# Kernel tuning notes

Measured on AMD Instinct MI355X. Metric: run time of the kernel, lower is better.

The kernel has to match this reference:

```python
import jax, jax.numpy as jnp
import numpy as np

N = 2048   # num_params = feature dim = number of ring Givens angles
B = 16384  # batch


def setup_inputs() -> dict:
    key = jax.random.key(0)
    k1, k2 = jax.random.split(key)
    x = jax.random.normal(k1, (B, N), dtype=jnp.float32)
    angles = jax.random.normal(k2, (N,), dtype=jnp.float32)
    return {"x": x, "angles": angles}


def _build_rotation(angles):
    """R = G_0 @ G_1 @ ... @ G_{n-1}, built by sequential right-multiplication.

    Right-multiplying M by Givens G_k (plane (i, j)=(k, (k+1)%n), angle theta_k,
    with G[i,i]=c, G[j,i]=s, G[i,j]=-s, G[j,j]=c) only mixes columns i and j:
        new_col_i =  c*col_i + s*col_j
        new_col_j = -s*col_i + c*col_j
    This is O(n) per step -> O(n^2) total, identical math to the original
    O(n^4) loop of full n x n matmuls against per-step identity matrices.
    """
    n = angles.shape[0]
    idx_i = jnp.arange(n)
    idx_j = (idx_i + 1) % n

    def step(M, inp):
        theta, i, j = inp
        c = jnp.cos(theta)
        s = jnp.sin(theta)
        col_i = M[:, i]
        col_j = M[:, j]
        M = M.at[:, i].set(c * col_i + s * col_j)
        M = M.at[:, j].set(-s * col_i + c * col_j)
        return M, None

    M0 = jnp.eye(n, dtype=angles.dtype)
    R, _ = jax.lax.scan(step, M0, (angles, idx_i, idx_j))
    return R


def reference(x, angles):
    R = _build_rotation(angles)   # [N, N], orthogonal (product of Givens)
    return x @ R.T                # [B, N]
```

## Files before the change

kernel.cpp:

```cpp
#include <hip/hip_runtime.h>
#include <stdint.h>

#define NN  2048
#define SEG 32
#define QPS 8
#define QPR 512
#define WPB 8
#define RPW 4

#define GLOBAL_AS __attribute__((address_space(1)))
#define LDS_AS    __attribute__((address_space(3)))

__global__ __launch_bounds__(512, 4) void ring_givens_scan_kernel(
        const float* __restrict__ x,
        const float* __restrict__ angles,
        float* __restrict__ y,
        int B) {
    __shared__ float4 csT2[SEG / 2][64];
    __shared__ float4 buf[WPB][QPR];
    const int tid  = threadIdx.x;
    const int lane = tid & 63;
    const int wib  = tid >> 6;
    float4* wl = buf[wib];

    {
        float4 av = ((const float4*)angles)[tid];
        float c0, s0, c1, s1, c2, s2, c3, s3;
        sincosf(av.x, &s0, &c0);
        sincosf(av.y, &s1, &c1);
        sincosf(av.z, &s2, &c2);
        sincosf(av.w, &s3, &c3);
        csT2[2 * (tid & 7)    ][tid >> 3] = make_float4(c0, s0, c1, s1);
        csT2[2 * (tid & 7) + 1][tid >> 3] = make_float4(c2, s2, c3, s3);
    }
    __syncthreads();

    const float4 csE = csT2[15][63];
    const float cl = csE.z, sl = csE.w;

    float Mseg = 1.0f;
    #pragma unroll
    for (int q = 0; q < QPS; ++q) {
        float4 A  = csT2[2 * q    ][lane];
        float4 Bq = csT2[2 * q + 1][lane];
        Mseg *= (A.y * A.w) * (Bq.y * Bq.w);
    }
    float Ms[6];
    float Mc = Mseg;
    #pragma unroll
    for (int d = 1, st = 0; d < 64; d <<= 1, ++st) {
        Ms[st] = (lane + d < 64) ? Mc : 0.0f;
        float Mo = __shfl_down(Mc, d);
        if (lane + d < 64) Mc = Mc * Mo;
    }
    float Mn = __shfl_down(Mc, 1);
    Mn = (lane == 63) ? 1.0f : Mn;

    const int gwid        = blockIdx.x * WPB + wib;
    const int total_waves = gridDim.x * WPB;

    for (int r = 0; r < RPW; ++r) {
        const int row = gwid + r * total_waves;
        if (row >= B) break;
        const float4* __restrict__ xr4 = (const float4*)(x + (size_t)row * NN);
        float4*       __restrict__ yr4 = (float4*)      (y + (size_t)row * NN);

        #pragma unroll
        for (int t = 0; t < 8; ++t) {
            const int srcq = (t * 64 + lane) ^ ((lane >> 3) & 7);
            __builtin_amdgcn_global_load_lds(
                (const GLOBAL_AS uint32_t*)(const void*)(xr4 + srcq),
                (LDS_AS uint32_t*)(void*)(wl + t * 64), 16, 0, 0);
        }
        asm volatile("s_waitcnt vmcnt(0)" ::: "memory");

        const float x0v = ((const float*)wl)[0];
        const float xlv = ((const float*)wl)[504 * 4 + 3];
        const float t0  = sl * xlv + cl * x0v;
        if (lane == 0) ((float*)wl)[0] = t0;

        float U = 0.0f;
        #pragma unroll
        for (int q = QPS - 1; q >= 0; --q) {
            float4 v  = wl[lane * QPS + (q ^ (lane & 7))];
            float4 A  = csT2[2 * q    ][lane];
            float4 Bq = csT2[2 * q + 1][lane];
            U = Bq.z * v.w - Bq.w * U;
            U = Bq.x * v.z - Bq.y * U;
            U = A.z  * v.y - A.w  * U;
            U = A.x  * v.x - A.y  * U;
        }

        #pragma unroll
        for (int d = 1, st = 0; d < 64; d <<= 1, ++st) {
            float Uo = __shfl_down(U, d);
            U = fmaf(Ms[st], Uo, U);
        }
        float Un = __shfl_down(U, 1);
        Un = (lane == 63) ? 0.0f : Un;
        float a = fmaf(Mn, x0v, Un);

        const int segq = lane * QPS;
        float e31, p0, p1, p2;
        {
            float4 v  = wl[segq + (7 ^ (lane & 7))];
            float4 A  = csT2[14][lane];
            float4 Bq = csT2[15][lane];
            e31 = Bq.w * v.w + Bq.z * a;  a = Bq.z * v.w - Bq.w * a;
            p2  = Bq.y * v.z + Bq.x * a;  a = Bq.x * v.z - Bq.y * a;
            p1  = A.w  * v.y + A.z  * a;  a = A.z  * v.y - A.w  * a;
            p0  = A.y  * v.x + A.x  * a;  a = A.x  * v.x - A.y  * a;
        }
        #pragma unroll
        for (int q = QPS - 2; q >= 0; --q) {
            float4 v  = wl[segq + (q ^ (lane & 7))];
            float4 A  = csT2[2 * q    ][lane];
            float4 Bq = csT2[2 * q + 1][lane];
            float e3 = Bq.w * v.w + Bq.z * a;  a = Bq.z * v.w - Bq.w * a;
            wl[segq + ((q + 1) ^ (lane & 7))] = make_float4(e3, p0, p1, p2);
            float e2 = Bq.y * v.z + Bq.x * a;  a = Bq.x * v.z - Bq.y * a;
            float e1 = A.w  * v.y + A.z  * a;  a = A.z  * v.y - A.w  * a;
            float e0 = A.y  * v.x + A.x  * a;  a = A.x  * v.x - A.y  * a;
            p0 = e0; p1 = e1; p2 = e2;
        }
        float prev = __shfl_up(e31, 1);
        float s0v  = (lane == 0) ? a : prev;
        wl[segq + (0 ^ (lane & 7))] = make_float4(s0v, p0, p1, p2);

        #pragma unroll
        for (int t = 0; t < 8; ++t) {
            const int p = t * 64 + lane;
            float4 v = wl[p ^ ((lane >> 3) & 7)];
            yr4[p] = v;
        }
        asm volatile("s_waitcnt lgkmcnt(0)" ::: "memory");
    }
}

extern "C" void kernel_launch(void* const* d_in, const int* in_sizes, int n_in,
                              void* d_out, int out_size, void* d_ws, size_t ws_size,
                              hipStream_t stream) {
    const float* x      = (const float*)d_in[0];
    const float* angles = (const float*)d_in[1];
    float* y            = (float*)d_out;

    const int B = in_sizes[0] / NN;
    const int total_waves = (B + RPW - 1) / RPW;
    const int blocks = (total_waves + WPB - 1) / WPB;
    hipLaunchKernelGGL(ring_givens_scan_kernel, dim3(blocks), dim3(512), 0, stream,
                       x, angles, y, B);
}
```

Measured before the change: 249.3 us.

## Double-buffer row loads into LDS and keep cos/sin coefficients in registers

Each wave now prefetches the next row into a second LDS buffer with async global-to-LDS loads while it computes the current row, so load latency overlaps with the scan. Cos/sin coefficients are computed per lane into registers instead of a shared LDS table, which removes the __syncthreads and the repeated LDS reads; the row segment is also read once into registers. The block shrinks to 4 waves and each wave handles 8 rows. This raises register pressure and LDS per wave, and relies on the vmcnt(8) count matching the store/load ordering; the trailing lgkmcnt wait was removed while LDS is reused across iterations.

```diff
diff --git a/kernel.cpp b/kernel.cpp
--- a/kernel.cpp
+++ b/kernel.cpp
@@ -2,49 +2,45 @@
 #include <stdint.h>
 
 #define NN  2048
-#define SEG 32
 #define QPS 8
 #define QPR 512
-#define WPB 8
-#define RPW 4
+#define WPB 4
+#define RPW 8
 
 #define GLOBAL_AS __attribute__((address_space(1)))
 #define LDS_AS    __attribute__((address_space(3)))
 
-__global__ __launch_bounds__(512, 4) void ring_givens_scan_kernel(
+__global__ __launch_bounds__(256, 2) void ring_givens_scan_kernel(
         const float* __restrict__ x,
         const float* __restrict__ angles,
         float* __restrict__ y,
         int B) {
-    __shared__ float4 csT2[SEG / 2][64];
-    __shared__ float4 buf[WPB][QPR];
-    const int tid  = threadIdx.x;
-    const int lane = tid & 63;
-    const int wib  = tid >> 6;
-    float4* wl = buf[wib];
+    __shared__ float4 buf[WPB][2][QPR];
+    const int lane = threadIdx.x & 63;
+    const int wib  = threadIdx.x >> 6;
+    float4* b0 = buf[wib][0];
+    float4* b1 = buf[wib][1];
 
+    float4 A[QPS], Bq[QPS];
     {
-        float4 av = ((const float4*)angles)[tid];
-        float c0, s0, c1, s1, c2, s2, c3, s3;
-        sincosf(av.x, &s0, &c0);
-        sincosf(av.y, &s1, &c1);
-        sincosf(av.z, &s2, &c2);
-        sincosf(av.w, &s3, &c3);
-        csT2[2 * (tid & 7)    ][tid >> 3] = make_float4(c0, s0, c1, s1);
-        csT2[2 * (tid & 7) + 1][tid >> 3] = make_float4(c2, s2, c3, s3);
+        const float4* ap4 = (const float4*)(angles + lane * 32);
+        #pragma unroll
+        for (int q = 0; q < QPS; ++q) {
+            float4 av = ap4[q];
+            float ss, cc;
+            sincosf(av.x, &ss, &cc); A[q].x = cc;  A[q].y = ss;
+            sincosf(av.y, &ss, &cc); A[q].z = cc;  A[q].w = ss;
+            sincosf(av.z, &ss, &cc); Bq[q].x = cc; Bq[q].y = ss;
+            sincosf(av.w, &ss, &cc); Bq[q].z = cc; Bq[q].w = ss;
+        }
     }
-    __syncthreads();
-
-    const float4 csE = csT2[15][63];
-    const float cl = csE.z, sl = csE.w;
+    float sl, cl;
+    sincosf(angles[NN - 1], &sl, &cl);
 
     float Mseg = 1.0f;
     #pragma unroll
-    for (int q = 0; q < QPS; ++q) {
-        float4 A  = csT2[2 * q    ][lane];
-        float4 Bq = csT2[2 * q + 1][lane];
-        Mseg *= (A.y * A.w) * (Bq.y * Bq.w);
-    }
+    for (int q = 0; q < QPS; ++q)
+        Mseg *= (A[q].y * A[q].w) * (Bq[q].y * Bq[q].w);
     float Ms[6];
     float Mc = Mseg;
     #pragma unroll
@@ -59,36 +55,56 @@
     const int gwid        = blockIdx.x * WPB + wib;
     const int total_waves = gridDim.x * WPB;
 
-    for (int r = 0; r < RPW; ++r) {
-        const int row = gwid + r * total_waves;
-        if (row >= B) break;
-        const float4* __restrict__ xr4 = (const float4*)(x + (size_t)row * NN);
-        float4*       __restrict__ yr4 = (float4*)      (y + (size_t)row * NN);
-
+    if (gwid < B) {
+        const float4* xr4 = (const float4*)(x + (size_t)gwid * NN);
         #pragma unroll
         for (int t = 0; t < 8; ++t) {
             const int srcq = (t * 64 + lane) ^ ((lane >> 3) & 7);
             __builtin_amdgcn_global_load_lds(
                 (const GLOBAL_AS uint32_t*)(const void*)(xr4 + srcq),
-                (LDS_AS uint32_t*)(void*)(wl + t * 64), 16, 0, 0);
+                (LDS_AS uint32_t*)(void*)(b0 + t * 64), 16, 0, 0);
         }
-        asm volatile("s_waitcnt vmcnt(0)" ::: "memory");
+    }
 
-        const float x0v = ((const float*)wl)[0];
-        const float xlv = ((const float*)wl)[504 * 4 + 3];
+    for (int r = 0; r < RPW; ++r) {
+        const int row = gwid + r * total_waves;
+        if (row >= B) break;
+        float4* P = (r & 1) ? b1 : b0;
+        float4* Q = (r & 1) ? b0 : b1;
+
+        if (r == 0) asm volatile("s_waitcnt vmcnt(0)" ::: "memory");
+        else        asm volatile("s_waitcnt vmcnt(8)" ::: "memory");
+
+        const int nrow = row + total_waves;
+        if (r + 1 < RPW && nrow < B) {
+            const float4* xn4 = (const float4*)(x + (size_t)nrow * NN);
+            #pragma unroll
+            for (int t = 0; t < 8; ++t) {
+                const int srcq = (t * 64 + lane) ^ ((lane >> 3) & 7);
+                __builtin_amdgcn_global_load_lds(
+                    (const GLOBAL_AS uint32_t*)(const void*)(xn4 + srcq),
+                    (LDS_AS uint32_t*)(void*)(Q + t * 64), 16, 0, 0);
+            }
+        }
+
+        const int segq = lane * QPS;
+        float4 w4[QPS];
+        #pragma unroll
+        for (int q = 0; q < QPS; ++q)
+            w4[q] = P[segq + (q ^ (lane & 7))];
+
+        const float x0v = __shfl(w4[0].x, 0);
+        const float xlv = __shfl(w4[7].w, 63);
         const float t0  = sl * xlv + cl * x0v;
-        if (lane == 0) ((float*)wl)[0] = t0;
+        if (lane == 0) w4[0].x = t0;
 
         float U = 0.0f;
         #pragma unroll
         for (int q = QPS - 1; q >= 0; --q) {
-            float4 v  = wl[lane * QPS + (q ^ (lane & 7))];
-            float4 A  = csT2[2 * q    ][lane];
-            float4 Bq = csT2[2 * q + 1][lane];
-            U = Bq.z * v.w - Bq.w * U;
-            U = Bq.x * v.z - Bq.y * U;
-            U = A.z  * v.y - A.w  * U;
-            U = A.x  * v.x - A.y  * U;
+            U = Bq[q].z * w4[q].w - Bq[q].w * U;
+            U = Bq[q].x * w4[q].z - Bq[q].y * U;
+            U = A[q].z  * w4[q].y - A[q].w  * U;
+            U = A[q].x  * w4[q].x - A[q].y  * U;
         }
 
         #pragma unroll
@@ -100,40 +116,35 @@
         Un = (lane == 63) ? 0.0f : Un;
         float a = fmaf(Mn, x0v, Un);
 
-        const int segq = lane * QPS;
         float e31, p0, p1, p2;
         {
-            float4 v  = wl[segq + (7 ^ (lane & 7))];
-            float4 A  = csT2[14][lane];
-            float4 Bq = csT2[15][lane];
-            e31 = Bq.w * v.w + Bq.z * a;  a = Bq.z * v.w - Bq.w * a;
-            p2  = Bq.y * v.z + Bq.x * a;  a = Bq.x * v.z - Bq.y * a;
-            p1  = A.w  * v.y + A.z  * a;  a = A.z  * v.y - A.w  * a;
-            p0  = A.y  * v.x + A.x  * a;  a = A.x  * v.x - A.y  * a;
+            float4 v = w4[7];
+            e31 = Bq[7].w * v.w + Bq[7].z * a;  a = Bq[7].z * v.w - Bq[7].w * a;
+            p2  = Bq[7].y * v.z + Bq[7].x * a;  a = Bq[7].x * v.z - Bq[7].y * a;
+            p1  = A[7].w  * v.y + A[7].z  * a;  a = A[7].z  * v.y - A[7].w  * a;
+            p0  = A[7].y  * v.x + A[7].x  * a;  a = A[7].x  * v.x - A[7].y  * a;
         }
         #pragma unroll
         for (int q = QPS - 2; q >= 0; --q) {
-            float4 v  = wl[segq + (q ^ (lane & 7))];
-            float4 A  = csT2[2 * q    ][lane];
-            float4 Bq = csT2[2 * q + 1][lane];
-            float e3 = Bq.w * v.w + Bq.z * a;  a = Bq.z * v.w - Bq.w * a;
-            wl[segq + ((q + 1) ^ (lane & 7))] = make_float4(e3, p0, p1, p2);
-            float e2 = Bq.y * v.z + Bq.x * a;  a = Bq.x * v.z - Bq.y * a;
-            float e1 = A.w  * v.y + A.z  * a;  a = A.z  * v.y - A.w  * a;
-            float e0 = A.y  * v.x + A.x  * a;  a = A.x  * v.x - A.y  * a;
+            float4 v = w4[q];
+            float e3 = Bq[q].w * v.w + Bq[q].z * a;  a = Bq[q].z * v.w - Bq[q].w * a;
+            P[segq + ((q + 1) ^ (lane & 7))] = make_float4(e3, p0, p1, p2);
+            float e2 = Bq[q].y * v.z + Bq[q].x * a;  a = Bq[q].x * v.z - Bq[q].y * a;
+            float e1 = A[q].w  * v.y + A[q].z  * a;  a = A[q].z  * v.y - A[q].w  * a;
+            float e0 = A[q].y  * v.x + A[q].x  * a;  a = A[q].x  * v.x - A[q].y  * a;
             p0 = e0; p1 = e1; p2 = e2;
         }
         float prev = __shfl_up(e31, 1);
         float s0v  = (lane == 0) ? a : prev;
-        wl[segq + (0 ^ (lane & 7))] = make_float4(s0v, p0, p1, p2);
+        P[segq + (0 ^ (lane & 7))] = make_float4(s0v, p0, p1, p2);
 
+        float4* __restrict__ yr4 = (float4*)(y + (size_t)row * NN);
         #pragma unroll
         for (int t = 0; t < 8; ++t) {
             const int p = t * 64 + lane;
-            float4 v = wl[p ^ ((lane >> 3) & 7)];
+            float4 v = P[p ^ ((lane >> 3) & 7)];
             yr4[p] = v;
         }
-        asm volatile("s_waitcnt lgkmcnt(0)" ::: "memory");
     }
 }
 
@@ -147,6 +158,6 @@
     const int B = in_sizes[0] / NN;
     const int total_waves = (B + RPW - 1) / RPW;
     const int blocks = (total_waves + WPB - 1) / WPB;
-    hipLaunchKernelGGL(ring_givens_scan_kernel, dim3(blocks), dim3(512), 0, stream,
+    hipLaunchKernelGGL(ring_givens_scan_kernel, dim3(blocks), dim3(256), 0, stream,
                        x, angles, y, B);
 }
```

New measurement: 238.2 us. -4.4%, faster.
